# Performance work log

Measured on AMD Instinct MI355X. Metric: run time of the kernel, lower is better.

Reference implementation:

```python
import jax, jax.numpy as jnp
import numpy as np

N_HEAD = 16


def _rope_tables(T, head_dim, dtype):
    # RotaryEmbedding buffers: freqs = outer(t, inv_freq), half-dim tables [T, head_dim//2]
    inv_freq = 1.0 / (10000.0 ** (jnp.arange(0, head_dim, 2, dtype=jnp.float32) / head_dim))
    freqs = jnp.arange(T, dtype=jnp.float32)[:, None] * inv_freq[None, :]
    return jnp.cos(freqs).astype(dtype), jnp.sin(freqs).astype(dtype)


def _apply_rotary(x, cos, sin):
    # x: [B,H,T,D]; cos/sin: [T,D//2] broadcast over B,H
    d = x.shape[-1] // 2
    x1, x2 = x[..., :d], x[..., d:]
    return jnp.concatenate([x1 * cos - x2 * sin, x2 * cos + x1 * sin], axis=-1)


def setup_inputs() -> dict:
    key = jax.random.key(0)
    k1, k2, k3 = jax.random.split(key, 3)
    B, T, C = 2, 2048, 2048
    x = jax.random.normal(k1, (B, T, C), dtype=jnp.float32)
    Wqkv = jax.random.normal(k2, (C, 3 * C), dtype=jnp.float32) * (1.0 / np.sqrt(C))
    Wproj = jax.random.normal(k3, (C, C), dtype=jnp.float32) * (1.0 / np.sqrt(C))
    return {"x": x, "Wqkv": Wqkv, "Wproj": Wproj}


def reference(x, Wqkv, Wproj):
    B, T, C = x.shape
    H = N_HEAD
    D = C // H
    qkv = (x @ Wqkv).reshape(B, T, 3, H, D)
    q, k, v = qkv[:, :, 0], qkv[:, :, 1], qkv[:, :, 2]  # [B,T,H,D]
    q = jnp.transpose(q, (0, 2, 1, 3))  # [B,H,T,D]
    k = jnp.transpose(k, (0, 2, 1, 3))
    v = jnp.transpose(v, (0, 2, 1, 3))
    cos, sin = _rope_tables(T, D, x.dtype)
    q = _apply_rotary(q, cos, sin)
    k = _apply_rotary(k, cos, sin)
    scale = 1.0 / np.sqrt(D)
    scores = jnp.einsum('bhqd,bhkd->bhqk', q, k) * scale
    causal = jnp.tril(jnp.ones((T, T), dtype=bool))
    scores = jnp.where(causal, scores, jnp.finfo(scores.dtype).min)
    attn = jax.nn.softmax(scores, axis=-1)
    out = jnp.einsum('bhqk,bhkd->bhqd', attn, v)
    out = jnp.transpose(out, (0, 2, 1, 3)).reshape(B, T, C)
    return out @ Wproj
```

## Files before the change

### kernel.cpp

```cpp
#include <hip/hip_runtime.h>
#include <hip/hip_bf16.h>

typedef short s16b;
using bf16x4 = __attribute__((ext_vector_type(4))) short;
using bf16x8 = __attribute__((ext_vector_type(8))) short;
using f32x4  = __attribute__((ext_vector_type(4))) float;

#define DEVINL __device__ __forceinline__

DEVINL float bf2f(short u) {
    union { float f; unsigned u; } x;
    x.u = ((unsigned)(unsigned short)u) << 16;
    return x.f;
}
DEVINL short f2bf(float f) {
    unsigned u = __builtin_bit_cast(unsigned, f);
    u += 0x7FFFu + ((u >> 16) & 1u);
    return (short)(u >> 16);
}

DEVINL f32x4 mfma16(bf16x8 a, bf16x8 b, f32x4 c) {
    return __builtin_amdgcn_mfma_f32_16x16x32_bf16(a, b, c, 0, 0, 0);
}

DEVINL void gload_lds16(const void* g, void* lds_uniform) {
    __builtin_amdgcn_global_load_lds(
        (const __attribute__((address_space(1))) char*)(const char*)g,
        (__attribute__((address_space(3))) char*)(char*)lds_uniform, 16, 0, 0);
}

DEVINL int perm32(int k) {
    return ((k >> 2) & 3) * 8 + ((k >> 4) & 1) * 4 + (k & 3);
}

DEVINL bf16x8 lds128(const s16b* base, int row, int ks, int g) {
    const char* p = (const char*)base + row * 128 + ((((ks << 2) + g) ^ (row & 7)) << 4);
    return *(const bf16x8*)p;
}
DEVINL bf16x8 lds256(const s16b* base, int row, int ds, int g) {
    const char* p = (const char*)base + row * 256 + ((((ds << 2) + g) ^ (row & 7)) << 4);
    return *(const bf16x8*)p;
}

__global__ void k_tables(float* __restrict__ ctab, float* __restrict__ stab) {
    int idx = blockIdx.x * 256 + threadIdx.x;
    int i = idx & 63, t = idx >> 6;
    float inv = powf(10000.0f, -(float)i * (1.0f / 64.0f));
    float fr = (float)t * inv;
    ctab[idx] = cosf(fr);
    stab[idx] = sinf(fr);
}

__global__ void k_cvt_x(const float* __restrict__ x, s16b* __restrict__ xb) {
    int idx = blockIdx.x * 256 + threadIdx.x;
    int p = idx * 4;
    int row = p >> 11, pc = p & 2047;
    int grp = pc >> 5, sp = pc & 31;
    int c = sp >> 3, half = (sp >> 2) & 1;
    int ksrc = grp * 32 + half * 16 + c * 4;
    float4 v = *(const float4*)(x + (size_t)row * 2048 + ksrc);
    bf16x4 o;
    o[0] = f2bf(v.x); o[1] = f2bf(v.y); o[2] = f2bf(v.z); o[3] = f2bf(v.w);
    *(bf16x4*)(xb + (size_t)row * 2048 + pc) = o;
}

__global__ void k_tcvt(const float* __restrict__ in, s16b* __restrict__ out, int R, int C) {
    __shared__ float tile[32][33];
    int tx = threadIdx.x & 31, ty = threadIdx.x >> 5;
    int c0 = blockIdx.x * 32, r0 = blockIdx.y * 32;
#pragma unroll
    for (int kk = 0; kk < 4; ++kk) {
        int r = ty + kk * 8;
        tile[r][tx] = in[(size_t)(r0 + r) * C + c0 + tx];
    }
    __syncthreads();
#pragma unroll
    for (int kk = 0; kk < 4; ++kk) {
        int r = ty + kk * 8;
        out[(size_t)(c0 + r) * R + r0 + perm32(tx)] = f2bf(tile[tx][r]);
    }
}

#define STG_B01(DB, KB)                                                        \
  gload_lds16(srcB + (KB), lds + 49152 + (DB) * 32768 + tid16);                \
  gload_lds16(srcB + 262144 + (KB), lds + 49152 + (DB) * 32768 + 8192 + tid16);
#define STG_B23(DB, KB)                                                        \
  gload_lds16(srcB + 524288 + (KB), lds + 49152 + (DB) * 32768 + 16384 + tid16); \
  gload_lds16(srcB + 786432 + (KB), lds + 49152 + (DB) * 32768 + 24576 + tid16);
#define STG_A01(DB, KB)                                                        \
  gload_lds16(srcA + (KB), lds + (DB) * 16384 + tid16);                        \
  gload_lds16(srcA + 262144 + (KB), lds + (DB) * 16384 + 8192 + tid16);

#define AF_READ(B, KS)                                                         \
    _Pragma("unroll")                                                          \
    for (int fi = 0; fi < 4; ++fi) {                                           \
      int row = (fi >> 1) * 64 + wm * 32 + (fi & 1) * 16 + r15;                \
      af[fi] = *(const bf16x8*)(lds + (B) * 16384 + row * 128                  \
               + ((((KS) * 4 + g) ^ (row & 7)) << 4));                         \
    }

#define PH4(B, KH, JH, STGC, WN)                                               \
  {                                                                            \
    if ((JH) == 0) { AF_READ(B, KH) }                                          \
    _Pragma("unroll")                                                          \
    for (int fj = 0; fj < 2; ++fj) {                                           \
      int row = (JH) * 128 + wn * 32 + fj * 16 + r15;                          \
      bfr[fj] = *(const bf16x8*)(lds + 49152 + (B) * 32768 + row * 128         \
                + ((((KH) * 4 + g) ^ (row & 7)) << 4));                        \
    }                                                                          \
    STGC                                                                       \
    if ((WN) == 6) { asm volatile("s_waitcnt vmcnt(6)" ::: "memory");          \
                     __builtin_amdgcn_sched_barrier(0); }                      \
    else if ((WN) == 0) { asm volatile("s_waitcnt vmcnt(0)" ::: "memory");     \
                     __builtin_amdgcn_sched_barrier(0); }                      \
    __builtin_amdgcn_s_barrier();                                              \
    asm volatile("s_waitcnt lgkmcnt(0)" ::: "memory");                         \
    __builtin_amdgcn_sched_barrier(0);                                         \
    __builtin_amdgcn_s_setprio(1);                                             \
    _Pragma("unroll")                                                          \
    for (int fi = 0; fi < 4; ++fi)                                             \
      _Pragma("unroll")                                                        \
      for (int fj = 0; fj < 2; ++fj)                                           \
        acc[fi][(JH) * 2 + fj] = mfma16(af[fi], bfr[fj], acc[fi][(JH) * 2 + fj]); \
    __builtin_amdgcn_s_setprio(0);                                             \
    __builtin_amdgcn_s_barrier();                                              \
    __builtin_amdgcn_sched_barrier(0);                                         \
  }

#define DO_TILE3(B, S1, S2, S3, WNL)                                           \
    PH4(B, 0, 0, S1, -1)                                                       \
    PH4(B, 0, 1, S2, -1)                                                       \
    PH4(B, 1, 0, S3, -1)                                                       \
    PH4(B, 1, 1, , WNL)

#define GEMM3_MAINLOOP(A_, B_)                                                 \
    __shared__ __attribute__((aligned(16))) char lds[147456];                  \
    const int tid = threadIdx.x;                                               \
    const int lane = tid & 63, wave = tid >> 6;                                \
    const int g = lane >> 4, r15 = lane & 15;                                  \
    const int wm = wave >> 2, wn = wave & 3;                                   \
    const int tid16 = tid << 4;                                                \
    const int rowL = tid16 >> 7;                                               \
    const int swzL = ((((tid16 >> 4) & 7) ^ (rowL & 7)) << 4);                 \
    const char* srcA = (const char*)(A_) + (size_t)(bm + rowL) * 4096 + swzL;  \
    const char* srcB = (const char*)(B_) + (size_t)(bn + rowL) * 4096 + swzL;  \
    f32x4 acc[4][4] = {};                                                      \
    bf16x8 af[4], bfr[2];                                                      \
    STG_B01(0, 0) STG_A01(0, 0) STG_B23(0, 0)                                  \
    STG_B01(1, 128) STG_A01(1, 128) STG_B23(1, 128)                            \
    asm volatile("s_waitcnt vmcnt(6)" ::: "memory");                           \
    __builtin_amdgcn_sched_barrier(0);                                         \
    __builtin_amdgcn_s_barrier();                                              \
    for (int t3 = 0; t3 < 10; ++t3) {                                          \
        const int kb2 = (3 * t3 + 2) * 128;                                    \
        const int kb3 = kb2 + 128, kb4 = kb2 + 256;                            \
        DO_TILE3(0, STG_B01(2, kb2), STG_A01(2, kb2), STG_B23(2, kb2), 6)      \
        DO_TILE3(1, STG_B01(0, kb3), STG_A01(0, kb3), STG_B23(0, kb3), 6)      \
        DO_TILE3(2, STG_B01(1, kb4), STG_A01(1, kb4), STG_B23(1, kb4), 6)      \
    }                                                                          \
    DO_TILE3(0, , , , 0)                                                       \
    DO_TILE3(1, , , , -1)

__global__ __launch_bounds__(512) void k_gemm_qkv(
    const s16b* __restrict__ A, const s16b* __restrict__ Bt,
    s16b* __restrict__ Qb, s16b* __restrict__ Kb, s16b* __restrict__ Vt) {
    const int bid = blockIdx.x;
    const int xcd = bid & 7, local = bid >> 3;
    const int rr_ = local >> 5, w = local & 31;
    const int bm = ((xcd & 3) * 8 + (w >> 2)) * 128;
    const int bn = ((xcd >> 2) * 12 + rr_ * 4 + (w & 3)) * 256;
    GEMM3_MAINLOOP(A, Bt)
    const int which = bn >> 11;
    if (which < 2) {
        s16b* dst = which ? Kb : Qb;
        char* sml = (char*)lds;
#pragma unroll
        for (int i = 0; i < 4; ++i) {
#pragma unroll
            for (int j = 0; j < 4; ++j) {
                int mb0 = (i >> 1) * 64 + wm * 32 + (i & 1) * 16 + 4 * g;
                int nn = (j >> 1) * 128 + wn * 32 + (j & 1) * 16 + r15;
#pragma unroll
                for (int e = 0; e < 4; ++e) {
                    int mm = mb0 + e;
                    *(s16b*)(sml + mm * 528 + ((nn * 2) ^ ((mm & 3) << 5))) =
                        f2bf(acc[i][j][e]);
                }
            }
        }
        __syncthreads();
        const int mrow = tid >> 2, c4 = tid & 3;
        const int bb = bm >> 11;
        const int tt = (bm & 2047) + mrow;
        const char* srow = sml + mrow * 528;
        const int sw = (mrow & 3) << 5;
#pragma unroll
        for (int k = 0; k < 8; ++k) {
            int lc = c4 + 4 * k;
            bf16x8 v = *(const bf16x8*)(srow + ((lc * 16) ^ sw));
            int ng = bn + lc * 8;
            int h = (ng >> 7) & 15, d = ng & 127;
            *(bf16x8*)(dst + ((size_t)(bb * 16 + h) * 2048 + tt) * 128 + d) = v;
        }
    } else {
#pragma unroll
        for (int i = 0; i < 4; ++i) {
            int m0 = bm + (i >> 1) * 64 + wm * 32 + (i & 1) * 16 + 4 * g;
            int b = m0 >> 11, t0 = m0 & 2047;
#pragma unroll
            for (int j = 0; j < 4; ++j) {
                int n = bn + (j >> 1) * 128 + wn * 32 + (j & 1) * 16 + r15;
                int h = (n >> 7) & 15, d = n & 127;
                size_t bh = (size_t)(b * 16 + h);
                int pt = (t0 & ~31) + perm32(t0 & 31);
                size_t base = (bh * 128 + d) * 2048 + pt;
                bf16x4 pk;
#pragma unroll
                for (int e = 0; e < 4; ++e) pk[e] = f2bf(acc[i][j][e]);
                *(bf16x4*)(Vt + base) = pk;
            }
        }
    }
}

__global__ __launch_bounds__(512) void k_gemm_proj(
    const s16b* __restrict__ A, const s16b* __restrict__ Bt, float* __restrict__ Co) {
    const int bid = blockIdx.x;
    const int xcd = bid & 7, local = bid >> 3;
    const int bm = (xcd * 4 + (local & 3)) * 128;
    const int bn = (local >> 2) * 256;
    GEMM3_MAINLOOP(A, Bt)
#pragma unroll
    for (int i = 0; i < 4; ++i) {
        int m0 = bm + (i >> 1) * 64 + wm * 32 + (i & 1) * 16 + 4 * g;
#pragma unroll
        for (int j = 0; j < 4; ++j) {
            int n = bn + (j >> 1) * 128 + wn * 32 + (j & 1) * 16 + r15;
#pragma unroll
            for (int e = 0; e < 4; ++e) Co[(size_t)(m0 + e) * 2048 + n] = acc[i][j][e];
        }
    }
}

__global__ void k_rope(s16b* __restrict__ Qb, const s16b* __restrict__ Kb,
                       s16b* __restrict__ Kp,
                       const float* __restrict__ ctab, const float* __restrict__ stab) {
    int idx = blockIdx.x * 256 + threadIdx.x;
    int i4 = idx & 15;
    int t = (idx >> 4) & 2047;
    int bh = (idx >> 15) & 31;
    int which = idx >> 20;
    int d = i4 * 4;
    const float* cp = ctab + t * 64 + d;
    const float* sp = stab + t * 64 + d;
    size_t rowoff = ((size_t)bh * 2048 + t) * 128;
    if (which == 0) {
        s16b* P = Qb + rowoff;
        bf16x4 a = *(bf16x4*)(P + d);
        bf16x4 bv = *(bf16x4*)(P + d + 64);
        bf16x4 ra, rb;
#pragma unroll
        for (int e = 0; e < 4; ++e) {
            float c = cp[e], s = sp[e];
            float x1 = bf2f(a[e]), x2 = bf2f(bv[e]);
            ra[e] = f2bf(x1 * c - x2 * s);
            rb[e] = f2bf(x2 * c + x1 * s);
        }
        *(bf16x4*)(P + d) = ra;
        *(bf16x4*)(P + d + 64) = rb;
    } else {
        const s16b* Pi = Kb + rowoff;
        s16b* Po = Kp + rowoff;
        bf16x4 a = *(const bf16x4*)(Pi + d);
        bf16x4 bv = *(const bf16x4*)(Pi + d + 64);
        bf16x4 ra, rb;
#pragma unroll
        for (int e = 0; e < 4; ++e) {
            float c = cp[e], s = sp[e];
            float x1 = bf2f(a[e]), x2 = bf2f(bv[e]);
            ra[e] = f2bf(x1 * c - x2 * s);
            rb[e] = f2bf(x2 * c + x1 * s);
        }
        int d2 = d + 64;
        int pd  = (d  & ~31) + perm32(d  & 31);
        int pd2 = (d2 & ~31) + perm32(d2 & 31);
        *(bf16x4*)(Po + pd) = ra;
        *(bf16x4*)(Po + pd2) = rb;
    }
}

__global__ __launch_bounds__(256) void k_attn(
    const s16b* __restrict__ Qb, const s16b* __restrict__ Kp,
    const s16b* __restrict__ Vt, s16b* __restrict__ AO) {
    __shared__ alignas(16) s16b Ks[64 * 128];
    __shared__ alignas(16) s16b Vs[128 * 64];
    const int tid = threadIdx.x;
    const int lane = tid & 63, wave = tid >> 6;
    const int g = lane >> 4, r15 = lane & 15;
    const int bh = blockIdx.x, qt = 15 - blockIdx.y;
    const int q0 = qt * 128 + wave * 32;
    const s16b* Qg = Qb + (size_t)bh * 2048 * 128;
    const char* Kg = (const char*)(Kp + (size_t)bh * 2048 * 128);
    const char* Vg = (const char*)(Vt + (size_t)bh * 128 * 2048);

    bf16x8 qf[2][4];
#pragma unroll
    for (int qs = 0; qs < 2; ++qs)
#pragma unroll
        for (int ds = 0; ds < 4; ++ds) {
            const s16b* p = Qg + (size_t)(q0 + qs * 16 + r15) * 128 + ds * 32 + 4 * g;
            bf16x4 lo = *(const bf16x4*)p;
            bf16x4 hi = *(const bf16x4*)(p + 16);
            qf[qs][ds] = __builtin_shufflevector(lo, hi, 0, 1, 2, 3, 4, 5, 6, 7);
        }

    f32x4 ot[8][2] = {};
    float m_s[2] = {-3e38f, -3e38f};
    float l_s[2] = {0.f, 0.f};
    const float scale = 0.0883883476483184f;

    const int ktiles = qt * 2 + 2;
    for (int kt = 0; kt < ktiles; ++kt) {
        const int k0 = kt * 64;
        __syncthreads();
#pragma unroll
        for (int rr = 0; rr < 4; ++rr) {
            int uo = (rr * 256 + wave * 64) * 16;
            int o = uo + lane * 16;
            {
                int row = o >> 8, sl = (o >> 4) & 15;
                int sg = (sl ^ (row & 7)) << 4;
                gload_lds16(Kg + (size_t)(k0 + row) * 256 + sg, (char*)Ks + uo);
            }
            {
                int row = o >> 7, sl = (o >> 4) & 7;
                int sg = (sl ^ (row & 7)) << 4;
                gload_lds16(Vg + (size_t)row * 4096 + (size_t)k0 * 2 + sg, (char*)Vs + uo);
            }
        }
        __syncthreads();

        if (k0 <= q0 + 31) {
            f32x4 st[4][2] = {};
            __builtin_amdgcn_s_setprio(1);
#pragma unroll
            for (int ds = 0; ds < 4; ++ds) {
#pragma unroll
                for (int ks = 0; ks < 4; ++ks) {
                    bf16x8 kf = lds256(Ks, ks * 16 + r15, ds, g);
#pragma unroll
                    for (int qs = 0; qs < 2; ++qs)
                        st[ks][qs] = mfma16(kf, qf[qs][ds], st[ks][qs]);
                }
            }
            __builtin_amdgcn_s_setprio(0);
#pragma unroll
            for (int ks = 0; ks < 4; ++ks)
#pragma unroll
                for (int qs = 0; qs < 2; ++qs)
#pragma unroll
                    for (int e = 0; e < 4; ++e) {
                        int kk = k0 + ks * 16 + 4 * g + e;
                        int qq = q0 + qs * 16 + r15;
                        float s = st[ks][qs][e] * scale;
                        st[ks][qs][e] = (kk <= qq) ? s : -3e38f;
                    }
            float sf[2];
#pragma unroll
            for (int qs = 0; qs < 2; ++qs) {
                float mx = -3e38f;
#pragma unroll
                for (int ks = 0; ks < 4; ++ks)
#pragma unroll
                    for (int e = 0; e < 4; ++e) mx = fmaxf(mx, st[ks][qs][e]);
                mx = fmaxf(mx, __shfl_xor(mx, 16));
                mx = fmaxf(mx, __shfl_xor(mx, 32));
                float mn = fmaxf(m_s[qs], mx);
                sf[qs] = __expf(m_s[qs] - mn);
                m_s[qs] = mn;
                float sum = 0.f;
#pragma unroll
                for (int ks = 0; ks < 4; ++ks)
#pragma unroll
                    for (int e = 0; e < 4; ++e) {
                        float p = __expf(st[ks][qs][e] - mn);
                        st[ks][qs][e] = p;
                        sum += p;
                    }
                sum += __shfl_xor(sum, 16);
                sum += __shfl_xor(sum, 32);
                l_s[qs] = l_s[qs] * sf[qs] + sum;
            }
            bf16x8 pb[2][2];
#pragma unroll
            for (int k2 = 0; k2 < 2; ++k2)
#pragma unroll
                for (int qs = 0; qs < 2; ++qs) {
                    bf16x8 f;
#pragma unroll
                    for (int jj = 0; jj < 8; ++jj)
                        f[jj] = f2bf(st[2 * k2 + (jj >> 2)][qs][jj & 3]);
                    pb[k2][qs] = f;
                }
#pragma unroll
            for (int d8 = 0; d8 < 8; ++d8)
#pragma unroll
                for (int qs = 0; qs < 2; ++qs)
#pragma unroll
                    for (int e = 0; e < 4; ++e) ot[d8][qs][e] *= sf[qs];
            __builtin_amdgcn_s_setprio(1);
#pragma unroll
            for (int k2 = 0; k2 < 2; ++k2)
#pragma unroll
                for (int d8 = 0; d8 < 8; ++d8) {
                    bf16x8 vf = lds128(Vs, d8 * 16 + r15, k2, g);
#pragma unroll
                    for (int qs = 0; qs < 2; ++qs)
                        ot[d8][qs] = mfma16(vf, pb[k2][qs], ot[d8][qs]);
                }
            __builtin_amdgcn_s_setprio(0);
        }
    }
    int b = bh >> 4, h = bh & 15;
#pragma unroll
    for (int qs = 0; qs < 2; ++qs) {
        float inv = 1.0f / l_s[qs];
        int q = q0 + qs * 16 + r15;
#pragma unroll
        for (int d8 = 0; d8 < 8; ++d8) {
            bf16x4 pk;
#pragma unroll
            for (int e = 0; e < 4; ++e) pk[e] = f2bf(ot[d8][qs][e] * inv);
            size_t off = ((size_t)(b * 2048 + q)) * 2048
                       + h * 128 + (d8 >> 1) * 32 + g * 8 + (d8 & 1) * 4;
            *(bf16x4*)(AO + off) = pk;
        }
    }
}

extern "C" void kernel_launch(void* const* d_in, const int* in_sizes, int n_in,
                              void* d_out, int out_size, void* d_ws, size_t ws_size,
                              hipStream_t stream) {
    const float* x = (const float*)d_in[0];
    const float* Wqkv = (const float*)d_in[1];
    const float* Wproj = (const float*)d_in[2];
    float* out = (float*)d_out;

    char* ws = (char*)d_ws;
    float* ctab = (float*)ws;
    float* stab = ctab + 2048 * 64;
    size_t off = 1048576;
    s16b* xb = (s16b*)(ws + off); off += 16777216;
    s16b* wqkvt = (s16b*)(ws + off); off += 25165824;
    s16b* wprojt = (s16b*)(ws + off); off += 8388608;
    s16b* Qb = (s16b*)(ws + off); off += 16777216;
    s16b* Kb = (s16b*)(ws + off); off += 16777216;
    s16b* Vt = (s16b*)(ws + off); off += 16777216;
    s16b* AO = xb;
    s16b* Kp = wqkvt;

    k_tables<<<dim3(512), dim3(256), 0, stream>>>(ctab, stab);
    k_cvt_x<<<dim3(8192), dim3(256), 0, stream>>>(x, xb);
    k_tcvt<<<dim3(192, 64), dim3(256), 0, stream>>>(Wqkv, wqkvt, 2048, 6144);
    k_tcvt<<<dim3(64, 64), dim3(256), 0, stream>>>(Wproj, wprojt, 2048, 2048);
    k_gemm_qkv<<<dim3(768), dim3(512), 0, stream>>>(xb, wqkvt, Qb, Kb, Vt);
    k_rope<<<dim3(8192), dim3(256), 0, stream>>>(Qb, Kb, Kp, ctab, stab);
    k_attn<<<dim3(32, 16), dim3(256), 0, stream>>>(Qb, Kp, Vt, AO);
    k_gemm_proj<<<dim3(256), dim3(512), 0, stream>>>(AO, wprojt, out);
}
```

Baseline: 270.2 us.

## Fuse RoPE into QKV GEMM epilogue and double-buffer attention K/V tiles

Rotary embedding for Q and K is now applied in the QKV GEMM epilogue, which writes the permuted K layout directly, so the standalone rope kernel and its extra read/write pass over Q and K are gone. The attention kernel double-buffers its K/V shared-memory tiles, prefetching the next tile with a partial vmcnt wait so loads overlap compute. Softmax uses exp2 with the log2(e) factor folded into the scale. Query-tile scheduling interleaves long and short causal tiles. In exchange, attention uses twice the LDS, which may cut occupancy, and the GEMM epilogue carries more registers and table loads.

```diff
diff --git a/kernel.cpp b/kernel.cpp
--- a/kernel.cpp
+++ b/kernel.cpp
@@ -163,7 +163,8 @@
 
 __global__ __launch_bounds__(512) void k_gemm_qkv(
     const s16b* __restrict__ A, const s16b* __restrict__ Bt,
-    s16b* __restrict__ Qb, s16b* __restrict__ Kb, s16b* __restrict__ Vt) {
+    s16b* __restrict__ Qb, s16b* __restrict__ Kp, s16b* __restrict__ Vt,
+    const float* __restrict__ ctab, const float* __restrict__ stab) {
     const int bid = blockIdx.x;
     const int xcd = bid & 7, local = bid >> 3;
     const int rr_ = local >> 5, w = local & 31;
@@ -172,7 +173,6 @@
     GEMM3_MAINLOOP(A, Bt)
     const int which = bn >> 11;
     if (which < 2) {
-        s16b* dst = which ? Kb : Qb;
         char* sml = (char*)lds;
 #pragma unroll
         for (int i = 0; i < 4; ++i) {
@@ -194,26 +194,73 @@
         const int tt = (bm & 2047) + mrow;
         const char* srow = sml + mrow * 528;
         const int sw = (mrow & 3) << 5;
+        bf16x8 v[8];
 #pragma unroll
         for (int k = 0; k < 8; ++k) {
             int lc = c4 + 4 * k;
-            bf16x8 v = *(const bf16x8*)(srow + ((lc * 16) ^ sw));
-            int ng = bn + lc * 8;
-            int h = (ng >> 7) & 15, d = ng & 127;
-            *(bf16x8*)(dst + ((size_t)(bb * 16 + h) * 2048 + tt) * 128 + d) = v;
+            v[k] = *(const bf16x8*)(srow + ((lc * 16) ^ sw));
+        }
+        float cs[2][8], sn[2][8];
+#pragma unroll
+        for (int j = 0; j < 2; ++j) {
+            int d0 = 8 * c4 + 32 * j;
+            const float* cp = ctab + tt * 64 + d0;
+            const float* sp = stab + tt * 64 + d0;
+            *(float4*)&cs[j][0] = *(const float4*)cp;
+            *(float4*)&cs[j][4] = *(const float4*)(cp + 4);
+            *(float4*)&sn[j][0] = *(const float4*)sp;
+            *(float4*)&sn[j][4] = *(const float4*)(sp + 4);
+        }
+        bf16x8 o[8];
+#pragma unroll
+        for (int hh = 0; hh < 2; ++hh)
+#pragma unroll
+            for (int j = 0; j < 2; ++j) {
+                int kl = hh * 4 + j, kh = kl + 2;
+                bf16x8 r1, r2;
+#pragma unroll
+                for (int e = 0; e < 8; ++e) {
+                    float c = cs[j][e], s = sn[j][e];
+                    float x1 = bf2f(v[kl][e]), x2 = bf2f(v[kh][e]);
+                    r1[e] = f2bf(x1 * c - x2 * s);
+                    r2[e] = f2bf(x2 * c + x1 * s);
+                }
+                o[kl] = r1; o[kh] = r2;
+            }
+        if (which == 0) {
+#pragma unroll
+            for (int k = 0; k < 8; ++k) {
+                int lc = c4 + 4 * k;
+                int ng = bn + lc * 8;
+                int h = (ng >> 7) & 15, d = ng & 127;
+                *(bf16x8*)(Qb + ((size_t)(bb * 16 + h) * 2048 + tt) * 128 + d) = o[k];
+            }
+        } else {
+#pragma unroll
+            for (int k = 0; k < 8; ++k) {
+                int lc = c4 + 4 * k;
+                int ng = bn + lc * 8;
+                int h = (ng >> 7) & 15, d = ng & 127;
+                size_t base = ((size_t)(bb * 16 + h) * 2048 + tt) * 128 + (d & ~31);
+                int w2 = d & 31;
+                bf16x4 lo, hi;
+#pragma unroll
+                for (int e = 0; e < 4; ++e) { lo[e] = o[k][e]; hi[e] = o[k][e + 4]; }
+                *(bf16x4*)(Kp + base + perm32(w2)) = lo;
+                *(bf16x4*)(Kp + base + perm32(w2 + 4)) = hi;
+            }
         }
     } else {
 #pragma unroll
         for (int i = 0; i < 4; ++i) {
             int m0 = bm + (i >> 1) * 64 + wm * 32 + (i & 1) * 16 + 4 * g;
             int b = m0 >> 11, t0 = m0 & 2047;
+            int pt = (t0 & ~31) + perm32(t0 & 31);
 #pragma unroll
             for (int j = 0; j < 4; ++j) {
                 int n = bn + (j >> 1) * 128 + wn * 32 + (j & 1) * 16 + r15;
                 int h = (n >> 7) & 15, d = n & 127;
-                size_t bh = (size_t)(b * 16 + h);
-                int pt = (t0 & ~31) + perm32(t0 & 31);
-                size_t base = (bh * 128 + d) * 2048 + pt;
+                size_t base = ((size_t)(b * 16 + h) * 128 + d) * 2048 + pt;
                 bf16x4 pk;
 #pragma unroll
                 for (int e = 0; e < 4; ++e) pk[e] = f2bf(acc[i][j][e]);
@@ -242,66 +289,44 @@
     }
 }
 
-__global__ void k_rope(s16b* __restrict__ Qb, const s16b* __restrict__ Kb,
-                       s16b* __restrict__ Kp,
-                       const float* __restrict__ ctab, const float* __restrict__ stab) {
-    int idx = blockIdx.x * 256 + threadIdx.x;
-    int i4 = idx & 15;
-    int t = (idx >> 4) & 2047;
-    int bh = (idx >> 15) & 31;
-    int which = idx >> 20;
-    int d = i4 * 4;
-    const float* cp = ctab + t * 64 + d;
-    const float* sp = stab + t * 64 + d;
-    size_t rowoff = ((size_t)bh * 2048 + t) * 128;
-    if (which == 0) {
-        s16b* P = Qb + rowoff;
-        bf16x4 a = *(bf16x4*)(P + d);
-        bf16x4 bv = *(bf16x4*)(P + d + 64);
-        bf16x4 ra, rb;
-#pragma unroll
-        for (int e = 0; e < 4; ++e) {
-            float c = cp[e], s = sp[e];
-            float x1 = bf2f(a[e]), x2 = bf2f(bv[e]);
-            ra[e] = f2bf(x1 * c - x2 * s);
-            rb[e] = f2bf(x2 * c + x1 * s);
-        }
-        *(bf16x4*)(P + d) = ra;
-        *(bf16x4*)(P + d + 64) = rb;
-    } else {
-        const s16b* Pi = Kb + rowoff;
-        s16b* Po = Kp + rowoff;
-        bf16x4 a = *(const bf16x4*)(Pi + d);
-        bf16x4 bv = *(const bf16x4*)(Pi + d + 64);
-        bf16x4 ra, rb;
-#pragma unroll
-        for (int e = 0; e < 4; ++e) {
-            float c = cp[e], s = sp[e];
-            float x1 = bf2f(a[e]), x2 = bf2f(bv[e]);
-            ra[e] = f2bf(x1 * c - x2 * s);
-            rb[e] = f2bf(x2 * c + x1 * s);
-        }
-        int d2 = d + 64;
-        int pd  = (d  & ~31) + perm32(d  & 31);
-        int pd2 = (d2 & ~31) + perm32(d2 & 31);
-        *(bf16x4*)(Po + pd) = ra;
-        *(bf16x4*)(Po + pd2) = rb;
-    }
-}
-
 __global__ __launch_bounds__(256) void k_attn(
     const s16b* __restrict__ Qb, const s16b* __restrict__ Kp,
     const s16b* __restrict__ Vt, s16b* __restrict__ AO) {
-    __shared__ alignas(16) s16b Ks[64 * 128];
-    __shared__ alignas(16) s16b Vs[128 * 64];
+    __shared__ alignas(16) s16b Ks[2][64 * 128];
+    __shared__ alignas(16) s16b Vs[2][128 * 64];
     const int tid = threadIdx.x;
     const int lane = tid & 63, wave = tid >> 6;
     const int g = lane >> 4, r15 = lane & 15;
-    const int bh = blockIdx.x, qt = 15 - blockIdx.y;
+    const int bh = blockIdx.x;
+    const int qt = (blockIdx.y < 8) ? (15 - (int)blockIdx.y) : ((int)blockIdx.y - 8);
     const int q0 = qt * 128 + wave * 32;
     const s16b* Qg = Qb + (size_t)bh * 2048 * 128;
     const char* Kg = (const char*)(Kp + (size_t)bh * 2048 * 128);
     const char* Vg = (const char*)(Vt + (size_t)bh * 128 * 2048);
+
+#define ASTG(BUF, KT)                                                          \
+    {                                                                          \
+      const int k0s = (KT) * 64;                                               \
+      _Pragma("unroll")                                                        \
+      for (int rr = 0; rr < 4; ++rr) {                                         \
+        int uo = (rr * 256 + wave * 64) * 16;                                  \
+        int o = uo + lane * 16;                                                \
+        {                                                                      \
+          int row = o >> 8, sl = (o >> 4) & 15;                                \
+          int sg = (sl ^ (row & 7)) << 4;                                      \
+          gload_lds16(Kg + (size_t)(k0s + row) * 256 + sg,                     \
+                      (char*)Ks + (BUF) * 16384 + uo);                         \
+        }                                                                      \
+        {                                                                      \
+          int row = o >> 7, sl = (o >> 4) & 7;                                 \
+          int sg = (sl ^ (row & 7)) << 4;                                      \
+          gload_lds16(Vg + (size_t)row * 4096 + (size_t)k0s * 2 + sg,          \
+                      (char*)Vs + (BUF) * 16384 + uo);                         \
+        }                                                                      \
+      }                                                                        \
+    }
+
+    ASTG(0, 0)
 
     bf16x8 qf[2][4];
 #pragma unroll
@@ -317,37 +342,32 @@
     f32x4 ot[8][2] = {};
     float m_s[2] = {-3e38f, -3e38f};
     float l_s[2] = {0.f, 0.f};
-    const float scale = 0.0883883476483184f;
+    const float scale2 = 0.12751744f;
 
     const int ktiles = qt * 2 + 2;
     for (int kt = 0; kt < ktiles; ++kt) {
         const int k0 = kt * 64;
-        __syncthreads();
-#pragma unroll
-        for (int rr = 0; rr < 4; ++rr) {
-            int uo = (rr * 256 + wave * 64) * 16;
-            int o = uo + lane * 16;
-            {
-                int row = o >> 8, sl = (o >> 4) & 15;
-                int sg = (sl ^ (row & 7)) << 4;
-                gload_lds16(Kg + (size_t)(k0 + row) * 256 + sg, (char*)Ks + uo);
-            }
-            {
-                int row = o >> 7, sl = (o >> 4) & 7;
-                int sg = (sl ^ (row & 7)) << 4;
-                gload_lds16(Vg + (size_t)row * 4096 + (size_t)k0 * 2 + sg, (char*)Vs + uo);
-            }
-        }
-        __syncthreads();
+        if (kt + 1 < ktiles) {
+            ASTG((kt + 1) & 1, kt + 1)
+            asm volatile("s_waitcnt vmcnt(8)" ::: "memory");
+        } else {
+            asm volatile("s_waitcnt vmcnt(0)" ::: "memory");
+        }
+        __builtin_amdgcn_sched_barrier(0);
+        __builtin_amdgcn_s_barrier();
+        asm volatile("" ::: "memory");
+        __builtin_amdgcn_sched_barrier(0);
 
         if (k0 <= q0 + 31) {
+            const s16b* Kb_ = (const s16b*)((const char*)Ks + (kt & 1) * 16384);
+            const s16b* Vb_ = (const s16b*)((const char*)Vs + (kt & 1) * 16384);
             f32x4 st[4][2] = {};
             __builtin_amdgcn_s_setprio(1);
 #pragma unroll
             for (int ds = 0; ds < 4; ++ds) {
 #pragma unroll
                 for (int ks = 0; ks < 4; ++ks) {
-                    bf16x8 kf = lds256(Ks, ks * 16 + r15, ds, g);
+                    bf16x8 kf = lds256(Kb_, ks * 16 + r15, ds, g);
 #pragma unroll
                     for (int qs = 0; qs < 2; ++qs)
                         st[ks][qs] = mfma16(kf, qf[qs][ds], st[ks][qs]);
@@ -362,7 +382,7 @@
                     for (int e = 0; e < 4; ++e) {
                         int kk = k0 + ks * 16 + 4 * g + e;
                         int qq = q0 + qs * 16 + r15;
-                        float s = st[ks][qs][e] * scale;
+                        float s = st[ks][qs][e] * scale2;
                         st[ks][qs][e] = (kk <= qq) ? s : -3e38f;
                     }
             float sf[2];
@@ -376,14 +396,14 @@
                 mx = fmaxf(mx, __shfl_xor(mx, 16));
                 mx = fmaxf(mx, __shfl_xor(mx, 32));
                 float mn = fmaxf(m_s[qs], mx);
-                sf[qs] = __expf(m_s[qs] - mn);
+                sf[qs] = exp2f(m_s[qs] - mn);
                 m_s[qs] = mn;
                 float sum = 0.f;
 #pragma unroll
                 for (int ks = 0; ks < 4; ++ks)
 #pragma unroll
                     for (int e = 0; e < 4; ++e) {
-                        float p = __expf(st[ks][qs][e] - mn);
+                        float p = exp2f(st[ks][qs][e] - mn);
                         st[ks][qs][e] = p;
                         sum += p;
                     }
@@ -413,13 +433,16 @@
             for (int k2 = 0; k2 < 2; ++k2)
 #pragma unroll
                 for (int d8 = 0; d8 < 8; ++d8) {
-                    bf16x8 vf = lds128(Vs, d8 * 16 + r15, k2, g);
+                    bf16x8 vf = lds128(Vb_, d8 * 16 + r15, k2, g);
 #pragma unroll
                     for (int qs = 0; qs < 2; ++qs)
                         ot[d8][qs] = mfma16(vf, pb[k2][qs], ot[d8][qs]);
                 }
             __builtin_amdgcn_s_setprio(0);
         }
+        asm volatile("" ::: "memory");
+        __builtin_amdgcn_sched_barrier(0);
+        __builtin_amdgcn_s_barrier();
     }
     int b = bh >> 4, h = bh & 15;
 #pragma unroll
@@ -436,6 +459,7 @@
             *(bf16x4*)(AO + off) = pk;
         }
     }
+#undef ASTG
 }
 
 extern "C" void kernel_launch(void* const* d_in, const int* in_sizes, int n_in,
@@ -454,17 +478,15 @@
     s16b* wqkvt = (s16b*)(ws + off); off += 25165824;
     s16b* wprojt = (s16b*)(ws + off); off += 8388608;
     s16b* Qb = (s16b*)(ws + off); off += 16777216;
-    s16b* Kb = (s16b*)(ws + off); off += 16777216;
+    s16b* Kp = (s16b*)(ws + off); off += 16777216;
     s16b* Vt = (s16b*)(ws + off); off += 16777216;
     s16b* AO = xb;
-    s16b* Kp = wqkvt;
 
     k_tables<<<dim3(512), dim3(256), 0, stream>>>(ctab, stab);
     k_cvt_x<<<dim3(8192), dim3(256), 0, stream>>>(x, xb);
     k_tcvt<<<dim3(192, 64), dim3(256), 0, stream>>>(Wqkv, wqkvt, 2048, 6144);
     k_tcvt<<<dim3(64, 64), dim3(256), 0, stream>>>(Wproj, wprojt, 2048, 2048);
-    k_gemm_qkv<<<dim3(768), dim3(512), 0, stream>>>(xb, wqkvt, Qb, Kb, Vt);
-    k_rope<<<dim3(8192), dim3(256), 0, stream>>>(Qb, Kb, Kp, ctab, stab);
+    k_gemm_qkv<<<dim3(768), dim3(512), 0, stream>>>(xb, wqkvt, Qb, Kp, Vt, ctab, stab);
     k_attn<<<dim3(32, 16), dim3(256), 0, stream>>>(Qb, Kp, Vt, AO);
     k_gemm_proj<<<dim3(256), dim3(512), 0, stream>>>(AO, wprojt, out);
 }
```

New measurement: 297.7 us. 1.1x slower.
